# Kernel optimization log

Measured on AMD Instinct MI355X. Metric: run time of the kernel, lower is better.

Reference implementation:

```python
import jax, jax.numpy as jnp
import numpy as np

N = 8192       # patients (nodes)
E = 262144     # edges per graph (avg degree 32)
DF = 128       # dim_final
SLOPE = 0.25   # leaky_relu negative slope


def _spmm(rows, cols, vals, dense):
    # out[i] = sum_{e: rows[e]==i} vals[e] * dense[cols[e]]  == sparse_adj @ dense
    return jax.ops.segment_sum(vals[:, None] * dense[cols], rows, num_segments=N)


def _branch(x, rows, cols, vals, w1, b1, w2, b2):
    # GraphGCN: gc1 -> leaky_relu -> (dropout: identity in eval) -> gc2 -> leaky_relu
    h = _spmm(rows, cols, vals, x @ w1) + b1
    h = jax.nn.leaky_relu(h, negative_slope=SLOPE)
    h = _spmm(rows, cols, vals, h @ w2) + b2
    return jax.nn.leaky_relu(h, negative_slope=SLOPE)


def setup_inputs() -> dict:
    key = jax.random.key(0)
    ks = jax.random.split(key, 40)
    i = 0

    def xav(k, shape):
        std = (2.0 / (shape[0] + shape[1])) ** 0.5
        return std * jax.random.normal(k, shape, dtype=jnp.float32)

    inp = {}
    feat_dims = {"RNAseq": 4096, "dnam": 4096, "cn": 4096, "mic": 1024}
    for name, d in feat_dims.items():
        inp[name] = jax.random.normal(ks[i], (N, d), dtype=jnp.float32); i += 1
    for g in range(1, 5):
        inp[f"rows{g}"] = jax.random.randint(ks[i], (E,), 0, N, dtype=jnp.int32); i += 1
        inp[f"cols{g}"] = jax.random.randint(ks[i], (E,), 0, N, dtype=jnp.int32); i += 1
        inp[f"vals{g}"] = jax.random.uniform(ks[i], (E,), dtype=jnp.float32); i += 1
    # per-branch params: (in_dim, hid_dim); suffixes r=RNAseq, d=meth, c=CN, m=miRNA
    specs = {"r": (4096, 512), "d": (4096, 512), "c": (4096, 512), "m": (1024, 256)}
    for s, (din, dh) in specs.items():
        inp[f"w1_{s}"] = xav(ks[i], (din, dh)); i += 1
        inp[f"b1_{s}"] = jnp.zeros((dh,), jnp.float32)
        inp[f"w2_{s}"] = xav(ks[i], (dh, DF)); i += 1
        inp[f"b2_{s}"] = jnp.zeros((DF,), jnp.float32)
    return inp


def reference(RNAseq, dnam, cn, mic,
              rows1, cols1, vals1, rows2, cols2, vals2,
              rows3, cols3, vals3, rows4, cols4, vals4,
              w1_r, b1_r, w2_r, b2_r,
              w1_d, b1_d, w2_d, b2_d,
              w1_c, b1_c, w2_c, b2_c,
              w1_m, b1_m, w2_m, b2_m):
    x_r = _branch(RNAseq, rows1, cols1, vals1, w1_r, b1_r, w2_r, b2_r)
    x_d = _branch(dnam,   rows2, cols2, vals2, w1_d, b1_d, w2_d, b2_d)
    x_c = _branch(cn,     rows3, cols3, vals3, w1_c, b1_c, w2_c, b2_c)
    x_m = _branch(mic,    rows4, cols4, vals4, w1_m, b1_m, w2_m, b2_m)
    return (x_r + x_d + x_c + x_m) / 4.0
```

## Files before the change

kernel.cpp:

```cpp
#include <hip/hip_runtime.h>

#define N_NODES 8192
#define N_EDGES 262144
#define SLOPE 0.25f

typedef __attribute__((ext_vector_type(8))) short bf16x8;
typedef __attribute__((ext_vector_type(4))) float f32x4;

__device__ __forceinline__ float lrelu(float x) { return x >= 0.f ? x : SLOPE * x; }

__device__ __forceinline__ unsigned short bf16_rne(float x) {
    unsigned u = __float_as_uint(x);
    return (unsigned short)((u + 0x7FFFu + ((u >> 16) & 1u)) >> 16);
}
__device__ __forceinline__ float bf2f(unsigned short h) {
    return __uint_as_float(((unsigned)h) << 16);
}
__device__ __forceinline__ bf16x8 pack8(const float4& a, const float4& b) {
    bf16x8 r;
    r[0] = (short)bf16_rne(a.x); r[1] = (short)bf16_rne(a.y);
    r[2] = (short)bf16_rne(a.z); r[3] = (short)bf16_rne(a.w);
    r[4] = (short)bf16_rne(b.x); r[5] = (short)bf16_rne(b.y);
    r[6] = (short)bf16_rne(b.z); r[7] = (short)bf16_rne(b.w);
    return r;
}

#define GLDS16(g, l)                                                              \
    __builtin_amdgcn_global_load_lds((const __attribute__((address_space(1))) void*)(g), \
                                     (__attribute__((address_space(3))) void*)(l), 16, 0, 0)

struct TransB { const float* W[4]; unsigned short* Th[4]; int K[4]; int N[4]; };

__global__ __launch_bounds__(256) void tsplit(TransB tb) {
    const int z = blockIdx.z;
    const int K = tb.K[z], N = tb.N[z];
    const int k0 = blockIdx.x * 32, n0 = blockIdx.y * 32;
    if (k0 >= K || n0 >= N) return;
    __shared__ float t[32][33];
    const int tx = threadIdx.x & 31, ty = threadIdx.x >> 5;
    const float* W = tb.W[z];
#pragma unroll
    for (int i = 0; i < 32; i += 8)
        t[ty + i][tx] = W[(size_t)(k0 + ty + i) * N + n0 + tx];
    __syncthreads();
#pragma unroll
    for (int i = 0; i < 32; i += 8) {
        const int n = ty + i;
        tb.Th[z][(size_t)(n0 + n) * K + k0 + tx] = bf16_rne(t[tx][n]);
    }
}

struct GemmB {
    const void* A[4];
    const unsigned short* Bh[4];
    unsigned short* C[4];
    int K[4];
    int NT[4];
};

template <int NF, int AF32>
__global__ __launch_bounds__(256, 2) void gemm_bf16s(GemmB gb) {
    constexpr int BGR = NF / 2;
    const int nwg = gridDim.x * gridDim.y * gridDim.z;
    int id = (blockIdx.z * gridDim.y + blockIdx.y) * gridDim.x + blockIdx.x;
    const int cpx = nwg >> 3;
    id = (id & 7) * cpx + (id >> 3);
    const int by = id % gridDim.y;
    const int rest = id / gridDim.y;
    const int bx = rest % gridDim.x;
    const int z = rest / gridDim.x;

    const int nt = gb.NT[z];
    if (by >= nt) return;
    const int K = gb.K[z];
    const int N = nt * (NF * 32);
    const float* __restrict__ Af = (const float*)gb.A[z];
    const unsigned short* __restrict__ Ab = (const unsigned short*)gb.A[z];
    const unsigned short* __restrict__ Bh = gb.Bh[z];
    unsigned short* __restrict__ C = gb.C[z];

    __shared__ unsigned short As[3 * 4096];
    __shared__ unsigned short Bs[3 * NF * 1024];
    const int tid = threadIdx.x;
    const int w = tid >> 6, lane = tid & 63;
    const int wm = w >> 1, wn = w & 1;
    const int bm0 = bx * 128, bn0 = by * (NF * 32);

    auto stageB = [&](int buf, int kt) {
        const int k0 = kt << 5;
#pragma unroll
        for (int i = 0; i < BGR; ++i) {
            const int f = (w * BGR + i) * 64 + lane;
            const int row = f >> 2, s = f & 3;
            const int kg = s ^ ((row >> 1) & 3);
            GLDS16(Bh + (size_t)(bn0 + row) * K + k0 + kg * 8,
                   &Bs[buf * (NF * 1024) + (w * BGR + i) * 512]);
        }
    };
    auto stageAglds = [&](int buf, int kt) {
        const int k0 = kt << 5;
#pragma unroll
        for (int i = 0; i < 2; ++i) {
            const int f = (w * 2 + i) * 64 + lane;
            const int row = f >> 2, s = f & 3;
            const int kg = s ^ ((row >> 1) & 3);
            GLDS16(Ab + (size_t)(bm0 + row) * K + k0 + kg * 8,
                   &As[buf * 4096 + (w * 2 + i) * 512]);
        }
    };
    auto issueA = [&](float4 (&ar)[2][2], int kt) {
        const int k0 = kt << 5;
#pragma unroll
        for (int i = 0; i < 2; ++i) {
            const int f = i * 256 + tid;
            const int row = f >> 2, s = f & 3;
            const int kg = s ^ ((row >> 1) & 3);
            const float* src = Af + (size_t)(bm0 + row) * K + k0 + kg * 8;
            ar[i][0] = *reinterpret_cast<const float4*>(src);
            ar[i][1] = *reinterpret_cast<const float4*>(src + 4);
        }
    };
    auto writeA = [&](float4 (&ar)[2][2], int buf) {
#pragma unroll
        for (int i = 0; i < 2; ++i)
            *reinterpret_cast<bf16x8*>(&As[buf * 4096 + (i * 256 + tid) * 8]) =
                pack8(ar[i][0], ar[i][1]);
    };

    f32x4 acc[4][NF];
#pragma unroll
    for (int mf = 0; mf < 4; ++mf)
#pragma unroll
        for (int nf = 0; nf < NF; ++nf) acc[mf][nf] = (f32x4){0.f, 0.f, 0.f, 0.f};

    const int nk = K >> 5;
    float4 aE[2][2], aO[2][2];

    if constexpr (AF32) {
        issueA(aE, 0); stageB(0, 0);
        issueA(aO, 1); stageB(1, 1);
        asm volatile("s_waitcnt vmcnt(12)" ::: "memory");
        writeA(aE, 0);
        asm volatile("s_waitcnt lgkmcnt(0)" ::: "memory");
    } else {
        stageAglds(0, 0); stageB(0, 0);
        stageAglds(1, 1); stageB(1, 1);
    }

    auto body = [&](int t, float4 (&iset)[2][2], float4 (&wset)[2][2]) {
        const int cb = t % 3;
        if (t + 2 < nk) {
            if constexpr (AF32) issueA(iset, t + 2);
            else stageAglds((t + 2) % 3, t + 2);
            stageB((t + 2) % 3, t + 2);
            if constexpr (AF32) asm volatile("s_waitcnt vmcnt(16)" ::: "memory");
            else asm volatile("s_waitcnt vmcnt(8)" ::: "memory");
        } else if (t + 1 < nk) {
            if constexpr (AF32) asm volatile("s_waitcnt vmcnt(8)" ::: "memory");
            else asm volatile("s_waitcnt vmcnt(4)" ::: "memory");
        } else {
            asm volatile("s_waitcnt vmcnt(0)" ::: "memory");
        }
        __builtin_amdgcn_s_barrier();
        __builtin_amdgcn_sched_barrier(0);

        if constexpr (AF32) {
            if (t + 1 < nk) {
                if (t + 2 < nk) asm volatile("s_waitcnt vmcnt(12)" ::: "memory");
                else asm volatile("s_waitcnt vmcnt(4)" ::: "memory");
                writeA(wset, (t + 1) % 3);
            }
        }

        const int kq = lane >> 4;
        bf16x8 a[4], b[NF];
#pragma unroll
        for (int mf = 0; mf < 4; ++mf) {
            const int r = wm * 64 + mf * 16 + (lane & 15);
            a[mf] = *reinterpret_cast<const bf16x8*>(
                &As[cb * 4096 + r * 32 + ((kq ^ ((r >> 1) & 3)) << 3)]);
        }
#pragma unroll
        for (int nf = 0; nf < NF; ++nf) {
            const int r = wn * (NF * 16) + nf * 16 + (lane & 15);
            b[nf] = *reinterpret_cast<const bf16x8*>(
                &Bs[cb * (NF * 1024) + r * 32 + ((kq ^ ((r >> 1) & 3)) << 3)]);
        }
        __builtin_amdgcn_s_setprio(1);
#pragma unroll
        for (int mf = 0; mf < 4; ++mf)
#pragma unroll
            for (int nf = 0; nf < NF; ++nf)
                acc[mf][nf] = __builtin_amdgcn_mfma_f32_16x16x32_bf16(a[mf], b[nf], acc[mf][nf], 0, 0, 0);
        __builtin_amdgcn_s_setprio(0);

        asm volatile("s_waitcnt lgkmcnt(0)" ::: "memory");
        __builtin_amdgcn_s_barrier();
    };

    for (int t = 0; t < nk; t += 2) {
        body(t, aE, aO);
        body(t + 1, aO, aE);
    }

    const int cr = (lane >> 4) * 4, cc = lane & 15;
#pragma unroll
    for (int mf = 0; mf < 4; ++mf)
#pragma unroll
        for (int nf = 0; nf < NF; ++nf)
#pragma unroll
            for (int j = 0; j < 4; ++j)
                C[(size_t)(bm0 + wm * 64 + mf * 16 + cr + j) * N + bn0 + wn * (NF * 16) + nf * 16 + cc] =
                    bf16_rne(acc[mf][nf][j]);
}

struct GraphPtrs {
    const int* r[4];
    const int* c[4];
    const float* v[4];
};

__global__ __launch_bounds__(256) void hist4(GraphPtrs p, int* __restrict__ cnt4) {
    const int g = blockIdx.y;
    const int e = blockIdx.x * 256 + threadIdx.x;
    atomicAdd(&cnt4[g * N_NODES + p.r[g][e]], 1);
}

__global__ __launch_bounds__(256) void scan4(const int* __restrict__ cnt4,
                                             int* __restrict__ rs4,
                                             int* __restrict__ cur4) {
    const int g = blockIdx.x;
    const int* cnt = cnt4 + g * N_NODES;
    int* row_start = rs4 + (size_t)g * (N_NODES + 1);
    int* cursor = cur4 + g * N_NODES;
    __shared__ int ssum[256];
    const int t = threadIdx.x;
    int local[32];
    int s = 0;
#pragma unroll
    for (int j = 0; j < 32; ++j) { local[j] = cnt[t * 32 + j]; s += local[j]; }
    ssum[t] = s;
    __syncthreads();
    for (int off = 1; off < 256; off <<= 1) {
        const int v = ssum[t];
        const int add = (t >= off) ? ssum[t - off] : 0;
        __syncthreads();
        ssum[t] = v + add;
        __syncthreads();
    }
    int run = (t == 0) ? 0 : ssum[t - 1];
#pragma unroll
    for (int j = 0; j < 32; ++j) {
        row_start[t * 32 + j] = run;
        cursor[t * 32 + j] = run;
        run += local[j];
    }
    if (t == 255) row_start[N_NODES] = run;
}

__global__ __launch_bounds__(256) void scatter4(GraphPtrs p, int* __restrict__ cur4,
                                                unsigned long long* __restrict__ pe4) {
    const int g = blockIdx.y;
    const int e = blockIdx.x * 256 + threadIdx.x;
    const int r = p.r[g][e];
    const int pos = atomicAdd(&cur4[g * N_NODES + r], 1);
    pe4[(size_t)g * N_EDGES + pos] =
        (unsigned long long)(unsigned)p.c[g][e] |
        ((unsigned long long)__float_as_uint(p.v[g][e]) << 32);
}

struct SpmmB {
    const int* rs[4];
    const unsigned long long* pe[4];
    const unsigned short* Y[4];
    const float* bi[4];
    unsigned short* H[4];
    int nc[4];
};

__global__ __launch_bounds__(256) void spmm_h1x(SpmmB sb) {
    const int id = blockIdx.x;
    const int xcd = id & 7;
    const int z = xcd >> 1;
    const int rb = ((id >> 3) << 1) + (id & 1);
    const int row = rb * 4 + (threadIdx.x >> 6);
    const int lane = threadIdx.x & 63;
    const int nc = sb.nc[z];
    const int* rs = sb.rs[z];
    const int s = rs[row], e1 = rs[row + 1];
    const unsigned long long* pe = sb.pe[z];
    const unsigned short* Y = sb.Y[z];
    const float* bi = sb.bi[z];

    if (nc == 512) {
        const int base = lane * 8;
        float acc[8];
#pragma unroll
        for (int j = 0; j < 8; ++j) acc[j] = 0.f;
        for (int e = s; e < e1; ++e) {
            const unsigned long long ev = pe[e];
            const float v = __uint_as_float((unsigned)(ev >> 32));
            const bf16x8 raw = *reinterpret_cast<const bf16x8*>(
                Y + (size_t)(unsigned)ev * 512 + base);
#pragma unroll
            for (int j = 0; j < 8; ++j)
                acc[j] = fmaf(v, bf2f((unsigned short)raw[j]), acc[j]);
        }
        bf16x8 vh;
#pragma unroll
        for (int j = 0; j < 8; ++j) vh[j] = (short)bf16_rne(lrelu(acc[j] + bi[base + j]));
        *reinterpret_cast<bf16x8*>(sb.H[z] + (size_t)row * 512 + base) = vh;
    } else {
        const int base = lane * 4;
        float acc[4];
#pragma unroll
        for (int j = 0; j < 4; ++j) acc[j] = 0.f;
        for (int e = s; e < e1; ++e) {
            const unsigned long long ev = pe[e];
            const float v = __uint_as_float((unsigned)(ev >> 32));
            const ushort4 raw = *reinterpret_cast<const ushort4*>(
                Y + (size_t)(unsigned)ev * 256 + base);
            acc[0] = fmaf(v, bf2f(raw.x), acc[0]);
            acc[1] = fmaf(v, bf2f(raw.y), acc[1]);
            acc[2] = fmaf(v, bf2f(raw.z), acc[2]);
            acc[3] = fmaf(v, bf2f(raw.w), acc[3]);
        }
        ushort4 vh;
        vh.x = bf16_rne(lrelu(acc[0] + bi[base + 0]));
        vh.y = bf16_rne(lrelu(acc[1] + bi[base + 1]));
        vh.z = bf16_rne(lrelu(acc[2] + bi[base + 2]));
        vh.w = bf16_rne(lrelu(acc[3] + bi[base + 3]));
        *reinterpret_cast<ushort4*>(sb.H[z] + (size_t)row * 256 + base) = vh;
    }
}

template <int NC>
__global__ __launch_bounds__(256) void spmm_h1(const int* __restrict__ rs,
                                               const unsigned long long* __restrict__ pe,
                                               const unsigned short* __restrict__ Y,
                                               const float* __restrict__ bi,
                                               unsigned short* __restrict__ Hd) {
    constexpr int PL = NC / 64;
    const int row = (blockIdx.x * 256 + threadIdx.x) >> 6;
    const int lane = threadIdx.x & 63;
    const int s = rs[row], e1 = rs[row + 1];
    const int base = lane * PL;
    float acc[PL];
#pragma unroll
    for (int j = 0; j < PL; ++j) acc[j] = 0.f;
    for (int e = s; e < e1; ++e) {
        const unsigned long long ev = pe[e];
        const float v = __uint_as_float((unsigned)(ev >> 32));
        const unsigned short* y = Y + (size_t)(unsigned)ev * NC + base;
        if constexpr (PL == 8) {
            const bf16x8 raw = *reinterpret_cast<const bf16x8*>(y);
#pragma unroll
            for (int j = 0; j < 8; ++j)
                acc[j] = fmaf(v, bf2f((unsigned short)raw[j]), acc[j]);
        } else {
            const ushort4 raw = *reinterpret_cast<const ushort4*>(y);
            acc[0] = fmaf(v, bf2f(raw.x), acc[0]);
            acc[1] = fmaf(v, bf2f(raw.y), acc[1]);
            acc[2] = fmaf(v, bf2f(raw.z), acc[2]);
            acc[3] = fmaf(v, bf2f(raw.w), acc[3]);
        }
    }
    unsigned short* H = Hd + (size_t)row * NC + base;
    if constexpr (PL == 8) {
        bf16x8 vh;
#pragma unroll
        for (int j = 0; j < 8; ++j) vh[j] = (short)bf16_rne(lrelu(acc[j] + bi[base + j]));
        *reinterpret_cast<bf16x8*>(H) = vh;
    } else {
        ushort4 vh;
        vh.x = bf16_rne(lrelu(acc[0] + bi[base + 0]));
        vh.y = bf16_rne(lrelu(acc[1] + bi[base + 1]));
        vh.z = bf16_rne(lrelu(acc[2] + bi[base + 2]));
        vh.w = bf16_rne(lrelu(acc[3] + bi[base + 3]));
        *reinterpret_cast<ushort4*>(H) = vh;
    }
}

struct Out4 { const float* b2[4]; };

__global__ __launch_bounds__(256) void spmm_out4(const int* __restrict__ rs4,
                                                 const unsigned long long* __restrict__ pe4,
                                                 const unsigned short* __restrict__ Y2all,
                                                 Out4 ob, float* __restrict__ out) {
    const int row = (blockIdx.x * 256 + threadIdx.x) >> 6;
    const int lane = threadIdx.x & 63;
    const int base = lane * 2;
    float r0 = 0.f, r1 = 0.f;
#pragma unroll
    for (int b = 0; b < 4; ++b) {
        const int* rs = rs4 + (size_t)b * (N_NODES + 1);
        const int s = rs[row], e1 = rs[row + 1];
        const unsigned long long* pe = pe4 + (size_t)b * N_EDGES;
        const unsigned short* Y = Y2all + (size_t)b * N_NODES * 128;
        float a0 = 0.f, a1 = 0.f;
        for (int e = s; e < e1; ++e) {
            const unsigned long long ev = pe[e];
            const float v = __uint_as_float((unsigned)(ev >> 32));
            const unsigned u = *reinterpret_cast<const unsigned*>(
                Y + (size_t)(unsigned)ev * 128 + base);
            a0 = fmaf(v, __uint_as_float(u << 16), a0);
            a1 = fmaf(v, __uint_as_float(u & 0xFFFF0000u), a1);
        }
        const float* bi = ob.b2[b];
        r0 += lrelu(a0 + bi[base]);
        r1 += lrelu(a1 + bi[base + 1]);
    }
    *reinterpret_cast<float2*>(out + (size_t)row * 128 + base) =
        make_float2(0.25f * r0, 0.25f * r1);
}

__global__ __launch_bounds__(256) void spmm_out1(const int* __restrict__ rs,
                                                 const unsigned long long* __restrict__ pe,
                                                 const unsigned short* __restrict__ Y,
                                                 const float* __restrict__ bias,
                                                 float* __restrict__ out, int first) {
    const int row = (blockIdx.x * 256 + threadIdx.x) >> 6;
    const int lane = threadIdx.x & 63;
    const int base = lane * 2;
    const int s = rs[row], e1 = rs[row + 1];
    float a0 = 0.f, a1 = 0.f;
    for (int e = s; e < e1; ++e) {
        const unsigned long long ev = pe[e];
        const float v = __uint_as_float((unsigned)(ev >> 32));
        const unsigned u = *reinterpret_cast<const unsigned*>(
            Y + (size_t)(unsigned)ev * 128 + base);
        a0 = fmaf(v, __uint_as_float(u << 16), a0);
        a1 = fmaf(v, __uint_as_float(u & 0xFFFF0000u), a1);
    }
    float r0 = 0.25f * lrelu(a0 + bias[base]);
    float r1 = 0.25f * lrelu(a1 + bias[base + 1]);
    float* o = out + (size_t)row * 128 + base;
    if (!first) {
        const float2 p = *reinterpret_cast<const float2*>(o);
        r0 += p.x;
        r1 += p.y;
    }
    *reinterpret_cast<float2*>(o) = make_float2(r0, r1);
}

extern "C" void kernel_launch(void* const* d_in, const int* in_sizes, int n_in,
                              void* d_out, int out_size, void* d_ws, size_t ws_size,
                              hipStream_t stream) {
    const float* X[4] = {(const float*)d_in[0], (const float*)d_in[1],
                         (const float*)d_in[2], (const float*)d_in[3]};
    GraphPtrs gp;
    for (int b = 0; b < 4; ++b) {
        gp.r[b] = (const int*)d_in[4 + 3 * b];
        gp.c[b] = (const int*)d_in[5 + 3 * b];
        gp.v[b] = (const float*)d_in[6 + 3 * b];
    }
    const float *w1[4], *b1[4], *w2[4], *b2[4];
    for (int b = 0; b < 4; ++b) {
        w1[b] = (const float*)d_in[16 + 4 * b + 0];
        b1[b] = (const float*)d_in[16 + 4 * b + 1];
        w2[b] = (const float*)d_in[16 + 4 * b + 2];
        b2[b] = (const float*)d_in[16 + 4 * b + 3];
    }
    const int din[4] = {4096, 4096, 4096, 1024};
    const int dh[4] = {512, 512, 512, 256};
    float* out = (float*)d_out;

    char* wsc = (char*)d_ws;
    size_t off = 0;
    auto carve = [&](size_t bytes) {
        void* p = wsc + off;
        off += (bytes + 255) & ~(size_t)255;
        return p;
    };
    int* cnt4 = (int*)carve((size_t)4 * N_NODES * 4);
    int* rs4 = (int*)carve((size_t)4 * (N_NODES + 1) * 4);
    int* cur4 = (int*)carve((size_t)4 * N_NODES * 4);
    unsigned long long* pe4 = (unsigned long long*)carve((size_t)4 * N_EDGES * 8);

    size_t tier1_base = off;
    unsigned short *W1h[4], *W2h[4], *Y1[4], *H1[4];
    for (int b = 0; b < 4; ++b) W1h[b] = (unsigned short*)carve((size_t)dh[b] * din[b] * 2);
    for (int b = 0; b < 4; ++b) W2h[b] = (unsigned short*)carve((size_t)128 * dh[b] * 2);
    for (int b = 0; b < 4; ++b) Y1[b] = (unsigned short*)carve((size_t)N_NODES * dh[b] * 2);
    for (int b = 0; b < 4; ++b) H1[b] = (unsigned short*)carve((size_t)N_NODES * dh[b] * 2);
    unsigned short* Y2all = (unsigned short*)carve((size_t)4 * N_NODES * 128 * 2);
    const bool tier1 = (off <= ws_size);
    unsigned short* Y2s[4];
    if (tier1) {
        for (int b = 0; b < 4; ++b) Y2s[b] = Y2all + (size_t)b * N_NODES * 128;
    } else {
        off = tier1_base;
        unsigned short* w1h = (unsigned short*)carve((size_t)512 * 4096 * 2);
        unsigned short* w2h = (unsigned short*)carve((size_t)128 * 512 * 2);
        unsigned short* y1 = (unsigned short*)carve((size_t)N_NODES * 512 * 2);
        unsigned short* h1 = (unsigned short*)carve((size_t)N_NODES * 512 * 2);
        unsigned short* y2 = (unsigned short*)carve((size_t)N_NODES * 128 * 2);
        for (int b = 0; b < 4; ++b) {
            W1h[b] = w1h; W2h[b] = w2h;
            Y1[b] = y1; H1[b] = h1; Y2s[b] = y2;
        }
    }

    hipMemsetAsync(cnt4, 0, (size_t)4 * N_NODES * sizeof(int), stream);
    {
        dim3 g(N_EDGES / 256, 4);
        hist4<<<g, 256, 0, stream>>>(gp, cnt4);
        scan4<<<4, 256, 0, stream>>>(cnt4, rs4, cur4);
        scatter4<<<g, 256, 0, stream>>>(gp, cur4, pe4);
    }

    if (tier1) {
        TransB t1;
        for (int b = 0; b < 4; ++b) {
            t1.W[b] = w1[b]; t1.Th[b] = W1h[b];
            t1.K[b] = din[b]; t1.N[b] = dh[b];
        }
        tsplit<<<dim3(128, 16, 4), 256, 0, stream>>>(t1);

        GemmB g1;
        for (int b = 0; b < 4; ++b) {
            g1.A[b] = X[b]; g1.Bh[b] = W1h[b];
            g1.C[b] = Y1[b]; g1.K[b] = din[b]; g1.NT[b] = dh[b] / 256;
        }
        gemm_bf16s<8, 1><<<dim3(64, 2, 4), 256, 0, stream>>>(g1);

        SpmmB s1;
        for (int b = 0; b < 4; ++b) {
            s1.rs[b] = rs4 + (size_t)b * (N_NODES + 1);
            s1.pe[b] = pe4 + (size_t)b * N_EDGES;
            s1.Y[b] = Y1[b]; s1.bi[b] = b1[b]; s1.H[b] = H1[b];
            s1.nc[b] = dh[b];
        }
        spmm_h1x<<<8192, 256, 0, stream>>>(s1);

        TransB t2;
        for (int b = 0; b < 4; ++b) {
            t2.W[b] = w2[b]; t2.Th[b] = W2h[b];
            t2.K[b] = dh[b]; t2.N[b] = 128;
        }
        tsplit<<<dim3(16, 4, 4), 256, 0, stream>>>(t2);

        GemmB g2;
        for (int b = 0; b < 4; ++b) {
            g2.A[b] = H1[b]; g2.Bh[b] = W2h[b];
            g2.C[b] = Y2s[b]; g2.K[b] = dh[b]; g2.NT[b] = 1;
        }
        gemm_bf16s<4, 0><<<dim3(64, 1, 4), 256, 0, stream>>>(g2);

        Out4 ob;
        for (int b = 0; b < 4; ++b) ob.b2[b] = b2[b];
        spmm_out4<<<N_NODES / 4, 256, 0, stream>>>(rs4, pe4, Y2all, ob, out);
    } else {
        for (int b = 0; b < 4; ++b) {
            TransB t1;
            t1.W[0] = w1[b]; t1.Th[0] = W1h[b];
            t1.K[0] = din[b]; t1.N[0] = dh[b];
            tsplit<<<dim3(din[b] / 32, dh[b] / 32, 1), 256, 0, stream>>>(t1);
            GemmB g1;
            g1.A[0] = X[b]; g1.Bh[0] = W1h[b];
            g1.C[0] = Y1[b]; g1.K[0] = din[b]; g1.NT[0] = dh[b] / 256;
            gemm_bf16s<8, 1><<<dim3(64, dh[b] / 256, 1), 256, 0, stream>>>(g1);
            if (dh[b] == 512)
                spmm_h1<512><<<N_NODES / 4, 256, 0, stream>>>(
                    rs4 + (size_t)b * (N_NODES + 1), pe4 + (size_t)b * N_EDGES,
                    Y1[b], b1[b], H1[b]);
            else
                spmm_h1<256><<<N_NODES / 4, 256, 0, stream>>>(
                    rs4 + (size_t)b * (N_NODES + 1), pe4 + (size_t)b * N_EDGES,
                    Y1[b], b1[b], H1[b]);
            TransB t2;
            t2.W[0] = w2[b]; t2.Th[0] = W2h[b];
            t2.K[0] = dh[b]; t2.N[0] = 128;
            tsplit<<<dim3(dh[b] / 32, 4, 1), 256, 0, stream>>>(t2);
            GemmB g2;
            g2.A[0] = H1[b]; g2.Bh[0] = W2h[b];
            g2.C[0] = Y2s[b]; g2.K[0] = dh[b]; g2.NT[0] = 1;
            gemm_bf16s<4, 0><<<dim3(64, 1, 1), 256, 0, stream>>>(g2);
            spmm_out1<<<N_NODES / 4, 256, 0, stream>>>(
                rs4 + (size_t)b * (N_NODES + 1), pe4 + (size_t)b * N_EDGES,
                Y2s[b], b2[b], out, b == 0);
        }
    }
}
```

Measured before the change: 526.7 us.

## Load GEMM A operand directly to registers and halve M tile

The A operand no longer goes through shared memory. Each wave loads its MFMA fragment rows straight from global memory into registers, converting to bf16 in-register when the input is fp32. The M tile shrinks from 128 to 64 rows, which doubles the grid, and launch bounds rise to 3 blocks per CU. This removes LDS staging and the extra barrier waits for A, but loses cross-wave reuse of A, issues less coalesced fragment-shaped global loads, and re-reads B twice as often.

```diff
diff --git a/kernel.cpp b/kernel.cpp
--- a/kernel.cpp
+++ b/kernel.cpp
@@ -59,7 +59,7 @@
 };
 
 template <int NF, int AF32>
-__global__ __launch_bounds__(256, 2) void gemm_bf16s(GemmB gb) {
+__global__ __launch_bounds__(256, 3) void gemm_bf16s(GemmB gb) {
     constexpr int BGR = NF / 2;
     const int nwg = gridDim.x * gridDim.y * gridDim.z;
     int id = (blockIdx.z * gridDim.y + blockIdx.y) * gridDim.x + blockIdx.x;
@@ -79,12 +79,12 @@
     const unsigned short* __restrict__ Bh = gb.Bh[z];
     unsigned short* __restrict__ C = gb.C[z];
 
-    __shared__ unsigned short As[3 * 4096];
     __shared__ unsigned short Bs[3 * NF * 1024];
     const int tid = threadIdx.x;
     const int w = tid >> 6, lane = tid & 63;
     const int wm = w >> 1, wn = w & 1;
-    const int bm0 = bx * 128, bn0 = by * (NF * 32);
+    const int m15 = lane & 15, kq = lane >> 4;
+    const int bm0 = bx * 64, bn0 = by * (NF * 32);
 
     auto stageB = [&](int buf, int kt) {
         const int k0 = kt << 5;
@@ -97,120 +97,98 @@
                    &Bs[buf * (NF * 1024) + (w * BGR + i) * 512]);
         }
     };
-    auto stageAglds = [&](int buf, int kt) {
+    auto issueAf = [&](float4 (&ar)[2][2], int kt) {
         const int k0 = kt << 5;
 #pragma unroll
-        for (int i = 0; i < 2; ++i) {
-            const int f = (w * 2 + i) * 64 + lane;
-            const int row = f >> 2, s = f & 3;
-            const int kg = s ^ ((row >> 1) & 3);
-            GLDS16(Ab + (size_t)(bm0 + row) * K + k0 + kg * 8,
-                   &As[buf * 4096 + (w * 2 + i) * 512]);
+        for (int mf = 0; mf < 2; ++mf) {
+            const float* src = Af + (size_t)(bm0 + wm * 32 + mf * 16 + m15) * K + k0 + kq * 8;
+            ar[mf][0] = *reinterpret_cast<const float4*>(src);
+            ar[mf][1] = *reinterpret_cast<const float4*>(src + 4);
         }
     };
-    auto issueA = [&](float4 (&ar)[2][2], int kt) {
+    auto issueAb = [&](bf16x8 (&ar)[2], int kt) {
         const int k0 = kt << 5;
 #pragma unroll
-        for (int i = 0; i < 2; ++i) {
-            const int f = i * 256 + tid;
-            const int row = f >> 2, s = f & 3;
-            const int kg = s ^ ((row >> 1) & 3);
-            const float* src = Af + (size_t)(bm0 + row) * K + k0 + kg * 8;
-            ar[i][0] = *reinterpret_cast<const float4*>(src);
-            ar[i][1] = *reinterpret_cast<const float4*>(src + 4);
-        }
+        for (int mf = 0; mf < 2; ++mf)
+            ar[mf] = *reinterpret_cast<const bf16x8*>(
+                Ab + (size_t)(bm0 + wm * 32 + mf * 16 + m15) * K + k0 + kq * 8);
     };
-    auto writeA = [&](float4 (&ar)[2][2], int buf) {
-#pragma unroll
-        for (int i = 0; i < 2; ++i)
-            *reinterpret_cast<bf16x8*>(&As[buf * 4096 + (i * 256 + tid) * 8]) =
-                pack8(ar[i][0], ar[i][1]);
-    };
-
-    f32x4 acc[4][NF];
-#pragma unroll
-    for (int mf = 0; mf < 4; ++mf)
+
+    f32x4 acc[2][NF];
+#pragma unroll
+    for (int mf = 0; mf < 2; ++mf)
 #pragma unroll
         for (int nf = 0; nf < NF; ++nf) acc[mf][nf] = (f32x4){0.f, 0.f, 0.f, 0.f};
 
     const int nk = K >> 5;
-    float4 aE[2][2], aO[2][2];
+    float4 aEf[2][2], aOf[2][2];
+    bf16x8 aEb[2], aOb[2];
 
     if constexpr (AF32) {
-        issueA(aE, 0); stageB(0, 0);
-        issueA(aO, 1); stageB(1, 1);
-        asm volatile("s_waitcnt vmcnt(12)" ::: "memory");
-        writeA(aE, 0);
-        asm volatile("s_waitcnt lgkmcnt(0)" ::: "memory");
+        stageB(0, 0); issueAf(aEf, 0);
+        stageB(1, 1); issueAf(aOf, 1);
     } else {
-        stageAglds(0, 0); stageB(0, 0);
-        stageAglds(1, 1); stageB(1, 1);
-    }
-
-    auto body = [&](int t, float4 (&iset)[2][2], float4 (&wset)[2][2]) {
+        stageB(0, 0); issueAb(aEb, 0);
+        stageB(1, 1); issueAb(aOb, 1);
+    }
+
+    auto body = [&](int t, float4 (&arf)[2][2], bf16x8 (&arb)[2]) {
         const int cb = t % 3;
         if (t + 2 < nk) {
-            if constexpr (AF32) issueA(iset, t + 2);
-            else stageAglds((t + 2) % 3, t + 2);
             stageB((t + 2) % 3, t + 2);
             if constexpr (AF32) asm volatile("s_waitcnt vmcnt(16)" ::: "memory");
+            else asm volatile("s_waitcnt vmcnt(12)" ::: "memory");
+        } else if (t + 1 < nk) {
+            if constexpr (AF32) asm volatile("s_waitcnt vmcnt(12)" ::: "memory");
             else asm volatile("s_waitcnt vmcnt(8)" ::: "memory");
-        } else if (t + 1 < nk) {
-            if constexpr (AF32) asm volatile("s_waitcnt vmcnt(8)" ::: "memory");
-            else asm volatile("s_waitcnt vmcnt(4)" ::: "memory");
         } else {
             asm volatile("s_waitcnt vmcnt(0)" ::: "memory");
         }
         __builtin_amdgcn_s_barrier();
         __builtin_amdgcn_sched_barrier(0);
 
+        bf16x8 a[2];
         if constexpr (AF32) {
-            if (t + 1 < nk) {
-                if (t + 2 < nk) asm volatile("s_waitcnt vmcnt(12)" ::: "memory");
-                else asm volatile("s_waitcnt vmcnt(4)" ::: "memory");
-                writeA(wset, (t + 1) % 3);
-            }
-        }
-
-        const int kq = lane >> 4;
-        bf16x8 a[4], b[NF];
-#pragma unroll
-        for (int mf = 0; mf < 4; ++mf) {
-            const int r = wm * 64 + mf * 16 + (lane & 15);
-            a[mf] = *reinterpret_cast<const bf16x8*>(
-                &As[cb * 4096 + r * 32 + ((kq ^ ((r >> 1) & 3)) << 3)]);
-        }
+            a[0] = pack8(arf[0][0], arf[0][1]);
+            a[1] = pack8(arf[1][0], arf[1][1]);
+            if (t + 2 < nk) issueAf(arf, t + 2);
+        } else {
+            a[0] = arb[0];
+            a[1] = arb[1];
+            if (t + 2 < nk) issueAb(arb, t + 2);
+        }
+
+        bf16x8 b[NF];
 #pragma unroll
         for (int nf = 0; nf < NF; ++nf) {
-            const int r = wn * (NF * 16) + nf * 16 + (lane & 15);
+            const int r = wn * (NF * 16) + nf * 16 + m15;
             b[nf] = *reinterpret_cast<const bf16x8*>(
                 &Bs[cb * (NF * 1024) + r * 32 + ((kq ^ ((r >> 1) & 3)) << 3)]);
         }
         __builtin_amdgcn_s_setprio(1);
 #pragma unroll
-        for (int mf = 0; mf < 4; ++mf)
+        for (int mf = 0; mf < 2; ++mf)
 #pragma unroll
             for (int nf = 0; nf < NF; ++nf)
                 acc[mf][nf] = __builtin_amdgcn_mfma_f32_16x16x32_bf16(a[mf], b[nf], acc[mf][nf], 0, 0, 0);
         __builtin_amdgcn_s_setprio(0);
 
-        asm volatile("s_waitcnt lgkmcnt(0)" ::: "memory");
         __builtin_amdgcn_s_barrier();
     };
 
     for (int t = 0; t < nk; t += 2) {
-        body(t, aE, aO);
-        body(t + 1, aO, aE);
-    }
-
-    const int cr = (lane >> 4) * 4, cc = lane & 15;
-#pragma unroll
-    for (int mf = 0; mf < 4; ++mf)
+        body(t, aEf, aEb);
+        body(t + 1, aOf, aOb);
+    }
+
+    const int cr = kq * 4, cc = m15;
+#pragma unroll
+    for (int mf = 0; mf < 2; ++mf)
 #pragma unroll
         for (int nf = 0; nf < NF; ++nf)
 #pragma unroll
             for (int j = 0; j < 4; ++j)
-                C[(size_t)(bm0 + wm * 64 + mf * 16 + cr + j) * N + bn0 + wn * (NF * 16) + nf * 16 + cc] =
+                C[(size_t)(bm0 + wm * 32 + mf * 16 + cr + j) * N + bn0 + wn * (NF * 16) + nf * 16 + cc] =
                     bf16_rne(acc[mf][nf][j]);
 }
 
@@ -522,7 +500,7 @@
             g1.A[b] = X[b]; g1.Bh[b] = W1h[b];
             g1.C[b] = Y1[b]; g1.K[b] = din[b]; g1.NT[b] = dh[b] / 256;
         }
-        gemm_bf16s<8, 1><<<dim3(64, 2, 4), 256, 0, stream>>>(g1);
+        gemm_bf16s<8, 1><<<dim3(128, 2, 4), 256, 0, stream>>>(g1);
 
         SpmmB s1;
         for (int b = 0; b < 4; ++b) {
@@ -545,7 +523,7 @@
             g2.A[b] = H1[b]; g2.Bh[b] = W2h[b];
             g2.C[b] = Y2s[b]; g2.K[b] = dh[b]; g2.NT[b] = 1;
         }
-        gemm_bf16s<4, 0><<<dim3(64, 1, 4), 256, 0, stream>>>(g2);
+        gemm_bf16s<4, 0><<<dim3(128, 1, 4), 256, 0, stream>>>(g2);
 
         Out4 ob;
         for (int b = 0; b < 4; ++b) ob.b2[b] = b2[b];
@@ -559,7 +537,7 @@
             GemmB g1;
             g1.A[0] = X[b]; g1.Bh[0] = W1h[b];
             g1.C[0] = Y1[b]; g1.K[0] = din[b]; g1.NT[0] = dh[b] / 256;
-            gemm_bf16s<8, 1><<<dim3(64, dh[b] / 256, 1), 256, 0, stream>>>(g1);
+            gemm_bf16s<8, 1><<<dim3(128, dh[b] / 256 ? dh[b] / 256 : 1, 1), 256, 0, stream>>>(g1);
             if (dh[b] == 512)
                 spmm_h1<512><<<N_NODES / 4, 256, 0, stream>>>(
                     rs4 + (size_t)b * (N_NODES + 1), pe4 + (size_t)b * N_EDGES,
@@ -575,7 +553,7 @@
             GemmB g2;
             g2.A[0] = H1[b]; g2.Bh[0] = W2h[b];
             g2.C[0] = Y2s[b]; g2.K[0] = dh[b]; g2.NT[0] = 1;
-            gemm_bf16s<4, 0><<<dim3(64, 1, 1), 256, 0, stream>>>(g2);
+            gemm_bf16s<4, 0><<<dim3(128, 1, 1), 256, 0, stream>>>(g2);
             spmm_out1<<<N_NODES / 4, 256, 0, stream>>>(
                 rs4 + (size_t)b * (N_NODES + 1), pe4 + (size_t)b * N_EDGES,
                 Y2s[b], b2[b], out, b == 0);
```

Result: slower. 838.7 us (+59.2%).
